# Optimization experiments

Measured on AMD Instinct MI355X. Metric: run time of the kernel, lower is better.

## Reference

```python
import jax, jax.numpy as jnp
import numpy as np
from jax import lax

B, C, H, W = 32, 3, 128, 128
HP, WP = 7, 7          # feature map after 4 stride-2 valid 3x3 convs on 128
GH, GW = 32, 32        # glimpse shape
BN_EPS = 1e-5


def _conv(x, w, b, stride):
    y = lax.conv_general_dilated(x, w, (stride, stride), 'VALID',
                                 dimension_numbers=('NCHW', 'OIHW', 'NCHW'))
    return y + b[None, :, None, None]


def _bn(x, g, be):
    # training-mode BatchNorm2d: biased batch stats over (N,H,W)
    m = x.mean(axis=(0, 2, 3), keepdims=True)
    v = ((x - m) ** 2).mean(axis=(0, 2, 3), keepdims=True)
    return g[None, :, None, None] * (x - m) * lax.rsqrt(v + BN_EPS) + be[None, :, None, None]


def setup_inputs() -> dict:
    key = jax.random.key(0)
    ks = jax.random.split(key, 16)
    def w_init(k, shape):
        fan_in = shape[1] * shape[2] * shape[3]
        return (jax.random.normal(k, shape, jnp.float32) / np.sqrt(fan_in)).astype(jnp.float32)
    chans = [3, 64, 64, 64, 64]
    inp = {}
    inp['img'] = jax.random.normal(ks[0], (B, C, H, W), jnp.float32)
    inp['eps_scale'] = jax.random.normal(ks[1], (B, HP, WP, 2), jnp.float32)
    inp['eps_shift'] = jax.random.normal(ks[2], (B, HP, WP, 2), jnp.float32)
    for i in range(4):
        inp[f'w{i+1}'] = w_init(ks[3 + i], (chans[i + 1], chans[i], 3, 3))
        inp[f'b{i+1}'] = jnp.zeros((chans[i + 1],), jnp.float32)
        inp[f'g{i+1}'] = jnp.ones((chans[i + 1],), jnp.float32)
        inp[f'be{i+1}'] = jnp.zeros((chans[i + 1],), jnp.float32)
    inp['wp'] = w_init(ks[10], (64, 64, 1, 1)); inp['bp'] = jnp.zeros((64,), jnp.float32)
    inp['wz'] = w_init(ks[11], (11, 64, 1, 1)); inp['bz'] = jnp.zeros((11,), jnp.float32)
    return inp


def reference(img, eps_scale, eps_shift,
              w1, b1, g1, be1, w2, b2, g2, be2,
              w3, b3, g3, be3, w4, b4, g4, be4,
              wp, bp, wz, bz):
    h = img
    for (w, b, g, be) in ((w1, b1, g1, be1), (w2, b2, g2, be2),
                          (w3, b3, g3, be3), (w4, b4, g4, be4)):
        h = jax.nn.elu(_bn(_conv(h, w, b, 2), g, be))
    feats = jax.nn.elu(_conv(h, wp, bp, 1))            # [B,64,HP,WP]

    # --- znet and latent splits (only scale/shift affect returned glimpses) ---
    Z = _conv(feats, wz, bz, 1).transpose(0, 2, 3, 1)  # [B,HP,WP,11]
    smean, slogstd = Z[..., 3:5], Z[..., 5:7]
    shmean, shlogstd = Z[..., 7:9], Z[..., 9:11]
    z_scale = smean + jax.nn.softplus(slogstd) * eps_scale
    z_shift = shmean + jax.nn.softplus(shlogstd) * eps_shift

    glimpse_hw = jnp.array([GH, GW], jnp.float32)
    image_hw = jnp.array([H, W], jnp.float32)
    fmap_hw = jnp.array([HP, WP], jnp.float32)
    scale_img = jax.nn.sigmoid(z_scale) * glimpse_hw / image_hw   # [B,HP,WP,2] (h,w)
    shift_img = jax.nn.sigmoid(z_shift) / fmap_hw                 # [B,HP,WP,2] (i,j)

    ii = jnp.arange(HP, dtype=jnp.float32) / HP
    jj = jnp.arange(WP, dtype=jnp.float32) / WP
    ij = jnp.stack(jnp.meshgrid(ii, jj, indexing='ij'), axis=-1)  # [HP,WP,2]
    center = (ij[None] + shift_img) * 2.0 - 1.0                   # [B,HP,WP,2] in [-1,1]

    K = HP * WP
    th = scale_img[..., 0].reshape(B, K)   # height scale
    tw = scale_img[..., 1].reshape(B, K)   # width scale
    tx = center[..., 0].reshape(B, K)      # row (y) center
    ty = center[..., 1].reshape(B, K)      # col (x) center

    # affine_grid (align_corners=False) base coords; theta = [[tw,0,ty],[0,th,tx]]
    xb = (2.0 * jnp.arange(GW, dtype=jnp.float32) + 1.0) / GW - 1.0
    yb = (2.0 * jnp.arange(GH, dtype=jnp.float32) + 1.0) / GH - 1.0
    ixn = tw[:, :, None, None] * xb[None, None, None, :] + ty[:, :, None, None]  # [B,K,1,GW]
    iyn = th[:, :, None, None] * yb[None, None, :, None] + tx[:, :, None, None]  # [B,K,GH,1]
    # normalized -> pixel coords (align_corners=False)
    px = jnp.broadcast_to(((ixn + 1.0) * W - 1.0) * 0.5, (B, K, GH, GW))
    py = jnp.broadcast_to(((iyn + 1.0) * H - 1.0) * 0.5, (B, K, GH, GW))

    def sample_one(im, pxb, pyb):
        # im [C,H,W]; pxb/pyb [K,GH,GW]; bilinear, zero padding
        x0 = jnp.floor(pxb); y0 = jnp.floor(pyb)
        wx1 = pxb - x0; wy1 = pyb - y0
        x0i = x0.astype(jnp.int32); y0i = y0.astype(jnp.int32)
        x1i = x0i + 1; y1i = y0i + 1
        def g(yi, xi):
            m = ((xi >= 0) & (xi < W) & (yi >= 0) & (yi < H)).astype(im.dtype)
            v = im[:, jnp.clip(yi, 0, H - 1), jnp.clip(xi, 0, W - 1)]  # [C,K,GH,GW]
            return v * m[None]
        return (g(y0i, x0i) * ((1 - wy1) * (1 - wx1))[None]
                + g(y0i, x1i) * ((1 - wy1) * wx1)[None]
                + g(y1i, x0i) * (wy1 * (1 - wx1))[None]
                + g(y1i, x1i) * (wy1 * wx1)[None])

    xs = jax.vmap(sample_one)(img, px, py)            # [B,C,K,GH,GW]
    return xs.transpose(0, 2, 1, 3, 4).reshape(B * K, C, GH, GW)
```

## Files before the change

kernel.cpp:

```cpp
#include <hip/hip_runtime.h>
#include <math.h>

#define BATCH 32

__device__ __forceinline__ float eluf(float v) { return v > 0.f ? v : expm1f(v); }
__device__ __forceinline__ float softplusf(float x) {
    return fmaxf(x, 0.f) + log1pf(expf(-fabsf(x)));
}
__device__ __forceinline__ float sigmoidf(float x) { return 1.f / (1.f + expf(-x)); }

template <int CIN, int HIN, int RSIN, int HOUT, int WOUT, int RSOUT, int G, int BLOCK>
__global__ __launch_bounds__(BLOCK, 4) void conv_kernel(
    const float* __restrict__ in, const float* __restrict__ w,
    const float* __restrict__ bias, float* __restrict__ out)
{
    const int b   = blockIdx.x;
    const int co0 = blockIdx.y * G;
    const int t   = threadIdx.x;
    const int px  = blockIdx.z * BLOCK + t;
    const bool active = px < HOUT * WOUT;
    const int p = active ? px : 0;
    const int y = p / WOUT, x = p % WOUT;

    const float* ib = in + (size_t)b * CIN * HIN * RSIN + (2 * y) * RSIN + 2 * x;

    float acc[G];
#pragma unroll
    for (int u = 0; u < G; ++u) acc[u] = bias[co0 + u];

#define LOADPAIR(dst, ci)                                                   \
    {                                                                       \
        _Pragma("unroll")                                                   \
        for (int h_ = 0; h_ < 2; ++h_) {                                    \
            const float* ip = ib + (size_t)((ci) + h_) * (HIN * RSIN);      \
            float2 a0 = *(const float2*)(ip);                               \
            float2 a1 = *(const float2*)(ip + RSIN);                        \
            float2 a2 = *(const float2*)(ip + 2 * RSIN);                    \
            float  c0 = ip[2];                                              \
            float  c1 = ip[RSIN + 2];                                       \
            float  c2 = ip[2 * RSIN + 2];                                   \
            dst[h_ * 9 + 0] = a0.x; dst[h_ * 9 + 1] = a0.y; dst[h_ * 9 + 2] = c0; \
            dst[h_ * 9 + 3] = a1.x; dst[h_ * 9 + 4] = a1.y; dst[h_ * 9 + 5] = c1; \
            dst[h_ * 9 + 6] = a2.x; dst[h_ * 9 + 7] = a2.y; dst[h_ * 9 + 8] = c2; \
        }                                                                   \
    }

#define FMAPAIR(src, ci)                                                    \
    {                                                                       \
        const float* wc = w + (size_t)co0 * CIN * 9 + (ci) * 9;             \
        _Pragma("unroll")                                                   \
        for (int u = 0; u < G; ++u)                                         \
            _Pragma("unroll")                                               \
            for (int k = 0; k < 18; ++k)                                    \
                acc[u] = fmaf(src[k], wc[(size_t)u * CIN * 9 + k], acc[u]); \
    }

    if constexpr (CIN == 3) {
        float pch[27];
#pragma unroll
        for (int h_ = 0; h_ < 3; ++h_) {
            const float* ip = ib + (size_t)h_ * (HIN * RSIN);
            float2 a0 = *(const float2*)(ip);
            float2 a1 = *(const float2*)(ip + RSIN);
            float2 a2 = *(const float2*)(ip + 2 * RSIN);
            pch[h_ * 9 + 0] = a0.x; pch[h_ * 9 + 1] = a0.y; pch[h_ * 9 + 2] = ip[2];
            pch[h_ * 9 + 3] = a1.x; pch[h_ * 9 + 4] = a1.y; pch[h_ * 9 + 5] = ip[RSIN + 2];
            pch[h_ * 9 + 6] = a2.x; pch[h_ * 9 + 7] = a2.y; pch[h_ * 9 + 8] = ip[2 * RSIN + 2];
        }
#pragma unroll
        for (int u = 0; u < G; ++u)
#pragma unroll
            for (int k = 0; k < 27; ++k)
                acc[u] = fmaf(pch[k], w[(size_t)(co0 + u) * 27 + k], acc[u]);
    } else {
        float pA[18], pB[18];
        LOADPAIR(pA, 0)
#pragma unroll 1
        for (int ci0 = 0; ci0 + 4 < CIN; ci0 += 4) {
            LOADPAIR(pB, ci0 + 2)
            FMAPAIR(pA, ci0)
            LOADPAIR(pA, ci0 + 4)
            FMAPAIR(pB, ci0 + 2)
        }
        LOADPAIR(pB, CIN - 2)
        FMAPAIR(pA, CIN - 4)
        FMAPAIR(pB, CIN - 2)
    }
#undef LOADPAIR
#undef FMAPAIR

    if (active) {
#pragma unroll
        for (int u = 0; u < G; ++u)
            out[((size_t)(b * 64 + co0 + u) * HOUT + y) * RSOUT + x] = acc[u];
    }
}

template <int PLANE_PAD, int RSOUT, int BPS>
__global__ __launch_bounds__(256) void stats_kernel(
    const float* __restrict__ h, float* __restrict__ partial)
{
    const int c = blockIdx.x, sp = blockIdx.y, t = threadIdx.x;
    constexpr int N4 = PLANE_PAD / 4;
    constexpr int Q  = RSOUT / 4;
    float s = 0.f, q = 0.f;
    for (int bb = sp * BPS; bb < (sp + 1) * BPS; ++bb) {
        const float4* pp = (const float4*)(h + (size_t)(bb * 64 + c) * PLANE_PAD);
        for (int i = t; i < N4; i += 256) {
            float4 v = pp[i];
            float w_ = ((i & (Q - 1)) == (Q - 1)) ? 0.f : v.w;
            s += v.x + v.y + v.z + w_;
            q += v.x * v.x + v.y * v.y + v.z * v.z + w_ * w_;
        }
    }
    __shared__ float ls[4], lq[4];
    const int lane = t & 63, wv = t >> 6;
#pragma unroll
    for (int off = 32; off > 0; off >>= 1) {
        s += __shfl_down(s, off);
        q += __shfl_down(q, off);
    }
    if (lane == 0) { ls[wv] = s; lq[wv] = q; }
    __syncthreads();
    if (t == 0) {
        s = ls[0] + ls[1] + ls[2] + ls[3];
        q = lq[0] + lq[1] + lq[2] + lq[3];
        partial[(sp * 64 + c) * 2 + 0] = s;
        partial[(sp * 64 + c) * 2 + 1] = q;
    }
}

template <int PLANE_PAD, int NREAL>
__global__ __launch_bounds__(256) void bnelu_kernel(
    float* __restrict__ h, const float* __restrict__ partial,
    const float* __restrict__ g, const float* __restrict__ be)
{
    __shared__ float sa[64], sb[64];
    const int t = threadIdx.x;
    if (t < 64) {
        float s = 0.f, q = 0.f;
#pragma unroll
        for (int k = 0; k < 8; ++k) {
            s += partial[(k * 64 + t) * 2 + 0];
            q += partial[(k * 64 + t) * 2 + 1];
        }
        constexpr float invN = 1.f / (float)(BATCH * NREAL);
        float m = s * invN;
        float var = fmaf(q, invN, -m * m);
        float a = g[t] * rsqrtf(var + 1e-5f);
        sa[t] = a;
        sb[t] = fmaf(-a, m, be[t]);
    }
    __syncthreads();

    const long long total4 = (long long)BATCH * 64 * PLANE_PAD / 4;
    float4* h4 = (float4*)h;
    for (long long i4 = (long long)blockIdx.x * 256 + t; i4 < total4;
         i4 += (long long)gridDim.x * 256) {
        int c = (int)((i4 * 4 / PLANE_PAD) & 63);
        float a = sa[c], bb = sb[c];
        float4 v = h4[i4];
        v.x = eluf(fmaf(a, v.x, bb));
        v.y = eluf(fmaf(a, v.y, bb));
        v.z = eluf(fmaf(a, v.z, bb));
        v.w = eluf(fmaf(a, v.w, bb));
        h4[i4] = v;
    }
}

__global__ __launch_bounds__(256) void head_kernel(
    const float* __restrict__ x4, const float* __restrict__ partial4,
    const float* __restrict__ g4, const float* __restrict__ be4,
    const float* __restrict__ wp, const float* __restrict__ bp,
    const float* __restrict__ wz, const float* __restrict__ bz,
    const float* __restrict__ eps_scale, const float* __restrict__ eps_shift,
    float* __restrict__ params)
{
    __shared__ float xs[64 * 49];
    __shared__ float fe[64 * 49];
    __shared__ float zz[11 * 49];
    __shared__ float ha[64], hb[64];
    const int b = blockIdx.x, t = threadIdx.x;

    if (t < 64) {
        float s = 0.f, q = 0.f;
#pragma unroll
        for (int k = 0; k < 8; ++k) {
            s += partial4[(k * 64 + t) * 2 + 0];
            q += partial4[(k * 64 + t) * 2 + 1];
        }
        constexpr float invN = 1.f / (float)(BATCH * 49);
        float m = s * invN;
        float var = fmaf(q, invN, -m * m);
        float a = g4[t] * rsqrtf(var + 1e-5f);
        ha[t] = a;
        hb[t] = fmaf(-a, m, be4[t]);
    }
    __syncthreads();

    for (int i = t; i < 64 * 49; i += 256) {
        int c = i / 49, p = i % 49;
        float v = x4[(size_t)b * 64 * 56 + c * 56 + (p / 7) * 8 + (p % 7)];
        xs[i] = eluf(fmaf(ha[c], v, hb[c]));
    }
    __syncthreads();

    for (int i = t; i < 64 * 49; i += 256) {
        int co = i / 49, p = i % 49;
        float a = bp[co];
        for (int ci = 0; ci < 64; ++ci) a = fmaf(xs[ci * 49 + p], wp[co * 64 + ci], a);
        fe[i] = eluf(a);
    }
    __syncthreads();

    for (int i = t; i < 11 * 49; i += 256) {
        int co = i / 49, p = i % 49;
        float a = bz[co];
        for (int ci = 0; ci < 64; ++ci) a = fmaf(fe[ci * 49 + p], wz[co * 64 + ci], a);
        zz[i] = a;
    }
    __syncthreads();

    if (t < 49) {
        const int i = t / 7, j = t % 7;
        float es0 = eps_scale[((size_t)b * 49 + t) * 2 + 0];
        float es1 = eps_scale[((size_t)b * 49 + t) * 2 + 1];
        float eh0 = eps_shift[((size_t)b * 49 + t) * 2 + 0];
        float eh1 = eps_shift[((size_t)b * 49 + t) * 2 + 1];
        float zs0 = zz[3 * 49 + t] + softplusf(zz[5 * 49 + t]) * es0;
        float zs1 = zz[4 * 49 + t] + softplusf(zz[6 * 49 + t]) * es1;
        float zh0 = zz[7 * 49 + t] + softplusf(zz[9 * 49 + t]) * eh0;
        float zh1 = zz[8 * 49 + t] + softplusf(zz[10 * 49 + t]) * eh1;
        float th = sigmoidf(zs0) * 0.25f;
        float tw = sigmoidf(zs1) * 0.25f;
        float tx = ((float)i / 7.0f + sigmoidf(zh0) / 7.0f) * 2.f - 1.f;
        float ty = ((float)j / 7.0f + sigmoidf(zh1) / 7.0f) * 2.f - 1.f;
        float4* pp = (float4*)params;
        pp[b * 49 + t] = make_float4(th, tw, tx, ty);
    }
}

__device__ __forceinline__ float tap(const float* __restrict__ im, int yy, int xx) {
    bool ok = (xx >= 0) & (xx < 128) & (yy >= 0) & (yy < 128);
    int yc = min(max(yy, 0), 127);
    int xc = min(max(xx, 0), 127);
    return ok ? im[yc * 128 + xc] : 0.f;
}

__global__ __launch_bounds__(256) void sampler_kernel(
    const float* __restrict__ img, const float* __restrict__ params,
    float* __restrict__ out)
{
    const int bk = blockIdx.x;
    const int b  = bk / 49;
    const float4 pr = ((const float4*)params)[bk];
    const float th = pr.x, tw = pr.y, tx = pr.z, ty = pr.w;

    for (int idx = threadIdx.x; idx < 3072; idx += 256) {
        const int c  = idx >> 10;
        const int gy = (idx >> 5) & 31;
        const int gx = idx & 31;
        float xb = (2.f * gx + 1.f) / 32.f - 1.f;
        float yb = (2.f * gy + 1.f) / 32.f - 1.f;
        float ixn = fmaf(tw, xb, ty);
        float iyn = fmaf(th, yb, tx);
        float px = ((ixn + 1.f) * 128.f - 1.f) * 0.5f;
        float py = ((iyn + 1.f) * 128.f - 1.f) * 0.5f;
        float x0f = floorf(px), y0f = floorf(py);
        float wx = px - x0f, wy = py - y0f;
        int x0 = (int)x0f, y0 = (int)y0f;
        const float* im = img + ((size_t)b * 3 + c) * 16384;
        float v00 = tap(im, y0, x0);
        float v01 = tap(im, y0, x0 + 1);
        float v10 = tap(im, y0 + 1, x0);
        float v11 = tap(im, y0 + 1, x0 + 1);
        float r = v00 * (1.f - wy) * (1.f - wx) + v01 * (1.f - wy) * wx +
                  v10 * wy * (1.f - wx)        + v11 * wy * wx;
        out[(size_t)bk * 3072 + idx] = r;
    }
}

extern "C" void kernel_launch(void* const* d_in, const int* in_sizes, int n_in,
                              void* d_out, int out_size, void* d_ws, size_t ws_size,
                              hipStream_t stream)
{
    const float* img       = (const float*)d_in[0];
    const float* eps_scale = (const float*)d_in[1];
    const float* eps_shift = (const float*)d_in[2];
    const float* w1 = (const float*)d_in[3],  *b1 = (const float*)d_in[4];
    const float* g1 = (const float*)d_in[5],  *be1 = (const float*)d_in[6];
    const float* w2 = (const float*)d_in[7],  *b2 = (const float*)d_in[8];
    const float* g2 = (const float*)d_in[9],  *be2 = (const float*)d_in[10];
    const float* w3 = (const float*)d_in[11], *b3 = (const float*)d_in[12];
    const float* g3 = (const float*)d_in[13], *be3 = (const float*)d_in[14];
    const float* w4 = (const float*)d_in[15], *b4 = (const float*)d_in[16];
    const float* g4 = (const float*)d_in[17], *be4 = (const float*)d_in[18];
    const float* wp = (const float*)d_in[19], *bp = (const float*)d_in[20];
    const float* wz = (const float*)d_in[21], *bz = (const float*)d_in[22];

    float* ws     = (float*)d_ws;
    float* params = ws;
    float* part1  = ws + 8192;
    float* part2  = ws + 9216;
    float* part3  = ws + 10240;
    float* part4  = ws + 11264;
    float* h1     = ws + 16384;
    float* h2     = h1 + (size_t)32 * 64 * 63 * 64;
    float* h3     = h2 + (size_t)32 * 64 * 31 * 32;
    float* h4     = h3 + (size_t)32 * 64 * 15 * 16;

    float* outp = (float*)d_out;

    conv_kernel<3, 128, 128, 63, 63, 64, 16, 256>
        <<<dim3(32, 4, 16), 256, 0, stream>>>(img, w1, b1, h1);
    stats_kernel<63 * 64, 64, 4><<<dim3(64, 8), 256, 0, stream>>>(h1, part1);
    bnelu_kernel<63 * 64, 63 * 63><<<2048, 256, 0, stream>>>(h1, part1, g1, be1);

    conv_kernel<64, 63, 64, 31, 31, 32, 8, 256>
        <<<dim3(32, 8, 4), 256, 0, stream>>>(h1, w2, b2, h2);
    stats_kernel<31 * 32, 32, 4><<<dim3(64, 8), 256, 0, stream>>>(h2, part2);
    bnelu_kernel<31 * 32, 31 * 31><<<1984, 256, 0, stream>>>(h2, part2, g2, be2);

    conv_kernel<64, 31, 32, 15, 15, 16, 8, 256>
        <<<dim3(32, 8, 1), 256, 0, stream>>>(h2, w3, b3, h3);
    stats_kernel<15 * 16, 16, 4><<<dim3(64, 8), 256, 0, stream>>>(h3, part3);
    bnelu_kernel<15 * 16, 15 * 15><<<480, 256, 0, stream>>>(h3, part3, g3, be3);

    conv_kernel<64, 15, 16, 7, 7, 8, 8, 64>
        <<<dim3(32, 8, 1), 64, 0, stream>>>(h3, w4, b4, h4);
    stats_kernel<7 * 8, 8, 4><<<dim3(64, 8), 256, 0, stream>>>(h4, part4);

    head_kernel<<<32, 256, 0, stream>>>(h4, part4, g4, be4, wp, bp, wz, bz,
                                        eps_scale, eps_shift, params);

    sampler_kernel<<<1568, 256, 0, stream>>>(img, params, outp);
}
```

Baseline: 236.7 us.

## Fuse BN+ELU of layer 1 into LDS-tiled conv2 and specialize conv1

Adds a dedicated conv1 kernel where each thread computes all 64 output channels, so every input patch is loaded once instead of once per channel group. Adds a conv2 kernel that stages row tiles of h1 in shared memory, applies layer-1 BatchNorm+ELU while loading, and computes 16 output channels per block. This removes the separate bnelu pass over the largest activation and lets neighbouring output pixels share input loads. The generic conv kernel is simplified to a per-channel loop with unroll 2, replacing the software-pipelined pair loads. Costs: 64 accumulators per thread in conv1 add register pressure, and conv2 synchronises on every group of 8 input channels.

```diff
diff --git a/kernel.cpp b/kernel.cpp
--- a/kernel.cpp
+++ b/kernel.cpp
@@ -8,6 +8,130 @@
     return fmaxf(x, 0.f) + log1pf(expf(-fabsf(x)));
 }
 __device__ __forceinline__ float sigmoidf(float x) { return 1.f / (1.f + expf(-x)); }
+
+__global__ __launch_bounds__(256, 2) void conv1_kernel(
+    const float* __restrict__ in, const float* __restrict__ w,
+    const float* __restrict__ bias, float* __restrict__ out)
+{
+    const int b  = blockIdx.x;
+    const int t  = threadIdx.x;
+    const int px = blockIdx.z * 256 + t;
+    const bool active = px < 63 * 63;
+    const int p = active ? px : 0;
+    const int y = p / 63, x = p % 63;
+
+    const float* ib = in + (size_t)b * 3 * 128 * 128 + (2 * y) * 128 + 2 * x;
+
+    float pch[27];
+#pragma unroll
+    for (int ci = 0; ci < 3; ++ci) {
+        const float* ip = ib + ci * 128 * 128;
+        float2 a0 = *(const float2*)(ip);
+        float2 a1 = *(const float2*)(ip + 128);
+        float2 a2 = *(const float2*)(ip + 256);
+        pch[ci * 9 + 0] = a0.x; pch[ci * 9 + 1] = a0.y; pch[ci * 9 + 2] = ip[2];
+        pch[ci * 9 + 3] = a1.x; pch[ci * 9 + 4] = a1.y; pch[ci * 9 + 5] = ip[130];
+        pch[ci * 9 + 6] = a2.x; pch[ci * 9 + 7] = a2.y; pch[ci * 9 + 8] = ip[258];
+    }
+
+    float acc[64];
+#pragma unroll
+    for (int u = 0; u < 64; ++u) acc[u] = bias[u];
+
+#pragma unroll
+    for (int u = 0; u < 64; ++u)
+#pragma unroll
+        for (int k = 0; k < 27; ++k)
+            acc[u] = fmaf(pch[k], w[u * 27 + k], acc[u]);
+
+    if (active) {
+#pragma unroll
+        for (int u = 0; u < 64; ++u)
+            out[((size_t)(b * 64 + u) * 63 + y) * 64 + x] = acc[u];
+    }
+}
+
+__global__ __launch_bounds__(256, 2) void conv2_kernel(
+    const float* __restrict__ h1, const float* __restrict__ part1,
+    const float* __restrict__ g1, const float* __restrict__ be1,
+    const float* __restrict__ w, const float* __restrict__ bias,
+    float* __restrict__ out)
+{
+    __shared__ float tile[8 * 17 * 68];
+    __shared__ float bna[64], bnb[64];
+
+    const int b   = blockIdx.x;
+    const int co0 = blockIdx.y * 16;
+    const int ty0 = blockIdx.z * 8;
+    const int t   = threadIdx.x;
+
+    if (t < 64) {
+        float s = 0.f, q = 0.f;
+#pragma unroll
+        for (int k = 0; k < 8; ++k) {
+            s += part1[(k * 64 + t) * 2 + 0];
+            q += part1[(k * 64 + t) * 2 + 1];
+        }
+        constexpr float invN = 1.f / (float)(BATCH * 63 * 63);
+        float m = s * invN;
+        float var = fmaf(q, invN, -m * m);
+        float a = g1[t] * rsqrtf(var + 1e-5f);
+        bna[t] = a;
+        bnb[t] = fmaf(-a, m, be1[t]);
+    }
+    __syncthreads();
+
+    const int ty = t >> 5, tx = t & 31;
+    const bool active = (tx < 31) && (ty0 + ty < 31);
+
+    float acc[16];
+#pragma unroll
+    for (int u = 0; u < 16; ++u) acc[u] = bias[co0 + u];
+
+#pragma unroll 1
+    for (int cc0 = 0; cc0 < 64; cc0 += 8) {
+#pragma unroll 1
+        for (int ch = 0; ch < 8; ++ch) {
+            const int ci = cc0 + ch;
+            const float a = bna[ci], bb = bnb[ci];
+            const float* src = h1 + (size_t)(b * 64 + ci) * (63 * 64);
+#pragma unroll 1
+            for (int i = t; i < 272; i += 256) {
+                int r = i >> 4, c4 = i & 15;
+                int gr = 2 * ty0 + r;
+                gr = gr > 62 ? 62 : gr;
+                float4 v = *(const float4*)(src + gr * 64 + c4 * 4);
+                v.x = eluf(fmaf(a, v.x, bb));
+                v.y = eluf(fmaf(a, v.y, bb));
+                v.z = eluf(fmaf(a, v.z, bb));
+                v.w = eluf(fmaf(a, v.w, bb));
+                *(float4*)&tile[ch * 1156 + r * 68 + c4 * 4] = v;
+            }
+        }
+        __syncthreads();
+#pragma unroll
+        for (int ch = 0; ch < 8; ++ch) {
+            const float* tp = &tile[ch * 1156 + (2 * ty) * 68 + 2 * tx];
+            float pch[9];
+            pch[0] = tp[0];   pch[1] = tp[1];   pch[2] = tp[2];
+            pch[3] = tp[68];  pch[4] = tp[69];  pch[5] = tp[70];
+            pch[6] = tp[136]; pch[7] = tp[137]; pch[8] = tp[138];
+            const float* wc = w + (size_t)co0 * 576 + (cc0 + ch) * 9;
+#pragma unroll
+            for (int u = 0; u < 16; ++u)
+#pragma unroll
+                for (int j = 0; j < 9; ++j)
+                    acc[u] = fmaf(pch[j], wc[u * 576 + j], acc[u]);
+        }
+        __syncthreads();
+    }
+
+    if (active) {
+#pragma unroll
+        for (int u = 0; u < 16; ++u)
+            out[((size_t)(b * 64 + co0 + u) * 31 + (ty0 + ty)) * 32 + tx] = acc[u];
+    }
+}
 
 template <int CIN, int HIN, int RSIN, int HOUT, int WOUT, int RSOUT, int G, int BLOCK>
 __global__ __launch_bounds__(BLOCK, 4) void conv_kernel(
@@ -28,66 +152,24 @@
 #pragma unroll
     for (int u = 0; u < G; ++u) acc[u] = bias[co0 + u];
 
-#define LOADPAIR(dst, ci)                                                   \
-    {                                                                       \
-        _Pragma("unroll")                                                   \
-        for (int h_ = 0; h_ < 2; ++h_) {                                    \
-            const float* ip = ib + (size_t)((ci) + h_) * (HIN * RSIN);      \
-            float2 a0 = *(const float2*)(ip);                               \
-            float2 a1 = *(const float2*)(ip + RSIN);                        \
-            float2 a2 = *(const float2*)(ip + 2 * RSIN);                    \
-            float  c0 = ip[2];                                              \
-            float  c1 = ip[RSIN + 2];                                       \
-            float  c2 = ip[2 * RSIN + 2];                                   \
-            dst[h_ * 9 + 0] = a0.x; dst[h_ * 9 + 1] = a0.y; dst[h_ * 9 + 2] = c0; \
-            dst[h_ * 9 + 3] = a1.x; dst[h_ * 9 + 4] = a1.y; dst[h_ * 9 + 5] = c1; \
-            dst[h_ * 9 + 6] = a2.x; dst[h_ * 9 + 7] = a2.y; dst[h_ * 9 + 8] = c2; \
-        }                                                                   \
-    }
-
-#define FMAPAIR(src, ci)                                                    \
-    {                                                                       \
-        const float* wc = w + (size_t)co0 * CIN * 9 + (ci) * 9;             \
-        _Pragma("unroll")                                                   \
-        for (int u = 0; u < G; ++u)                                         \
-            _Pragma("unroll")                                               \
-            for (int k = 0; k < 18; ++k)                                    \
-                acc[u] = fmaf(src[k], wc[(size_t)u * CIN * 9 + k], acc[u]); \
-    }
-
-    if constexpr (CIN == 3) {
-        float pch[27];
-#pragma unroll
-        for (int h_ = 0; h_ < 3; ++h_) {
-            const float* ip = ib + (size_t)h_ * (HIN * RSIN);
-            float2 a0 = *(const float2*)(ip);
-            float2 a1 = *(const float2*)(ip + RSIN);
-            float2 a2 = *(const float2*)(ip + 2 * RSIN);
-            pch[h_ * 9 + 0] = a0.x; pch[h_ * 9 + 1] = a0.y; pch[h_ * 9 + 2] = ip[2];
-            pch[h_ * 9 + 3] = a1.x; pch[h_ * 9 + 4] = a1.y; pch[h_ * 9 + 5] = ip[RSIN + 2];
-            pch[h_ * 9 + 6] = a2.x; pch[h_ * 9 + 7] = a2.y; pch[h_ * 9 + 8] = ip[2 * RSIN + 2];
-        }
+#pragma unroll 2
+    for (int ci = 0; ci < CIN; ++ci) {
+        const float* ip = ib + (size_t)ci * (HIN * RSIN);
+        float2 a0 = *(const float2*)(ip);
+        float2 a1 = *(const float2*)(ip + RSIN);
+        float2 a2 = *(const float2*)(ip + 2 * RSIN);
+        float  c0 = ip[2];
+        float  c1 = ip[RSIN + 2];
+        float  c2 = ip[2 * RSIN + 2];
+        const float pch[9] = {a0.x, a0.y, c0, a1.x, a1.y, c1, a2.x, a2.y, c2};
+
+        const float* wc = w + ((size_t)co0 * CIN + ci) * 9;
 #pragma unroll
         for (int u = 0; u < G; ++u)
 #pragma unroll
-            for (int k = 0; k < 27; ++k)
-                acc[u] = fmaf(pch[k], w[(size_t)(co0 + u) * 27 + k], acc[u]);
-    } else {
-        float pA[18], pB[18];
-        LOADPAIR(pA, 0)
-#pragma unroll 1
-        for (int ci0 = 0; ci0 + 4 < CIN; ci0 += 4) {
-            LOADPAIR(pB, ci0 + 2)
-            FMAPAIR(pA, ci0)
-            LOADPAIR(pA, ci0 + 4)
-            FMAPAIR(pB, ci0 + 2)
-        }
-        LOADPAIR(pB, CIN - 2)
-        FMAPAIR(pA, CIN - 4)
-        FMAPAIR(pB, CIN - 2)
-    }
-#undef LOADPAIR
-#undef FMAPAIR
+            for (int j = 0; j < 9; ++j)
+                acc[u] = fmaf(pch[j], wc[u * CIN * 9 + j], acc[u]);
+    }
 
     if (active) {
 #pragma unroll
@@ -311,13 +393,10 @@
 
     float* outp = (float*)d_out;
 
-    conv_kernel<3, 128, 128, 63, 63, 64, 16, 256>
-        <<<dim3(32, 4, 16), 256, 0, stream>>>(img, w1, b1, h1);
+    conv1_kernel<<<dim3(32, 1, 16), 256, 0, stream>>>(img, w1, b1, h1);
     stats_kernel<63 * 64, 64, 4><<<dim3(64, 8), 256, 0, stream>>>(h1, part1);
-    bnelu_kernel<63 * 64, 63 * 63><<<2048, 256, 0, stream>>>(h1, part1, g1, be1);
-
-    conv_kernel<64, 63, 64, 31, 31, 32, 8, 256>
-        <<<dim3(32, 8, 4), 256, 0, stream>>>(h1, w2, b2, h2);
+
+    conv2_kernel<<<dim3(32, 4, 4), 256, 0, stream>>>(h1, part1, g1, be1, w2, b2, h2);
     stats_kernel<31 * 32, 32, 4><<<dim3(64, 8), 256, 0, stream>>>(h2, part2);
     bnelu_kernel<31 * 32, 31 * 31><<<1984, 256, 0, stream>>>(h2, part2, g2, be2);
 
```

After: 341.4 us. 1.44x slower.
